# Kernel optimization log

Hardware: AMD Instinct MI355X
Metric: run time of the kernel (lower is better)

The kernel has to match this reference:

```python
import jax, jax.numpy as jnp
import numpy as np

B, CIN, CE, CA, N, S = 2, 64, 128, 128, 1024, 32
SCALE = np.sqrt(np.float32(CA))  # scale_mode == 'dimfts'


def _vnlin(W, x):
    # VNLinear: linear map over the channel dim of (B, C, 3, N, S)
    return jnp.einsum('oc,bcdns->bodns', W, x)


def setup_inputs() -> dict:
    key = jax.random.key(0)
    ks = jax.random.split(key, 16)
    def w(k, o, i):
        return (jax.random.normal(k, (o, i), jnp.float32) / np.sqrt(np.float32(i)))
    return {
        'group_xyz': jax.random.normal(ks[0], (B, N, S, 3), jnp.float32),
        'group_fts': jax.random.normal(ks[1], (B, CIN, 3, N, S), jnp.float32),
        'query_xyz': jax.random.normal(ks[2], (B, N, 3), jnp.float32),
        'W_e1': w(ks[3], CE, CIN), 'W_e2': w(ks[4], CE, CE),
        'W_q': w(ks[5], CA, CE), 'W_k': w(ks[6], CA, CE), 'W_v': w(ks[7], CA, CE),
        'W_r1': w(ks[8], 64, 1), 'W_r2': w(ks[9], CA, 64),
        'W_std': w(ks[10], 3, CA),
        'W_f1': w(ks[11], CA, CA * 3), 'b_f1': jax.random.normal(ks[12], (CA,), jnp.float32) * 0.02,
        'W_f2': w(ks[13], CA, CA), 'b_f2': jax.random.normal(ks[14], (CA,), jnp.float32) * 0.02,
    }


def reference(group_xyz, group_fts, query_xyz, W_e1, W_e2, W_q, W_k, W_v,
              W_r1, W_r2, W_std, W_f1, b_f1, W_f2, b_f2):
    # vnn_e: two stacked VNLinear layers
    group_emb = _vnlin(W_e2, _vnlin(W_e1, group_fts))        # (B, CE, 3, N, S)
    query_emb = group_emb[..., :1]                           # (B, CE, 3, N, 1)
    q = _vnlin(W_q, query_emb)                               # (B, CA, 3, N, 1)
    k = _vnlin(W_k, group_emb)                               # (B, CA, 3, N, S)
    v = _vnlin(W_v, group_emb)                               # (B, CA, 3, N, S)

    # positional relation: xyz_rel -> (B, 1, 3, N, S) -> vnn_r
    xyz_rel = group_xyz - query_xyz[:, :, None, :]           # (B, N, S, 3)
    xyz_rel = jnp.transpose(xyz_rel[:, :, :, None, :], (0, 3, 4, 1, 2))  # (B,1,3,N,S)
    pos_rel = _vnlin(W_r2, _vnlin(W_r1, xyz_rel))            # (B, CA, 3, N, S)

    # relation_func == 'sub'
    attn = q - k + pos_rel                                   # (B, CA, 3, N, S)

    # VNStdFeatureLin (dim=5, no frame normalization): z0 = VNLinear(CA->3)
    z0 = _vnlin(W_std, attn)                                 # (B, 3, 3, N, S)
    attn = jnp.einsum('bijns,bjkns->bikns', attn, z0)        # (B, CA, 3, N, S) invariant

    # attn_fwd: 1x1 conv -> ReLU -> 1x1 conv on (B, CA*3, N, S)
    attn = attn.reshape(B, CA * 3, N, S)
    h = jax.nn.relu(jnp.einsum('oc,bcns->bons', W_f1, attn) + b_f1[:, None, None])
    a = jnp.einsum('oc,bcns->bons', W_f2, h) + b_f2[:, None, None]  # (B, CA, N, S)

    a = jax.nn.softmax(a[:, :, None, :, :] / SCALE, axis=-1)  # (B, CA, 1, N, S)
    v = v + pos_rel
    resi = jnp.sum(a * v, axis=-1)                            # (B, CA, 3, N)
    return resi
```

## Files before the change

kernel.cpp:

```cpp
#include <hip/hip_runtime.h>
#include <hip/hip_bf16.h>
#include <math.h>

typedef __hip_bfloat16  bf16;
typedef __hip_bfloat162 bf162;
typedef __attribute__((ext_vector_type(8))) short short8;
typedef __attribute__((ext_vector_type(4))) float f32x4;

#define BB   2
#define CINC 64
#define NN   1024
#define SSS  32
#define NS   (NN * SSS)

#define OFF_WE21 0
#define OFF_WR   8192
#define OFF_KBA  8320
#define OFF_VB   16512
#define OFF_F1B  20608
#define OFF_F2B  45184
#define WS_NEED_FLOATS 53376

#define S_ATT_B  0
#define S_FTS_B  26112
#define S_XYZ_B  39936
#define SMEM_BYTES 40128

__device__ __forceinline__ float bf2f(short s) {
    unsigned int u = ((unsigned int)(unsigned short)s) << 16;
    return __uint_as_float(u);
}
__device__ __forceinline__ short f2bf(float f) {
    bf16 h = __float2bfloat16(f);
    return *reinterpret_cast<short*>(&h);
}
__device__ __forceinline__ unsigned pk2(float a, float b) {
    bf162 p = __float22bfloat162_rn(make_float2(a, b));
    return *reinterpret_cast<unsigned*>(&p);
}

__global__ __launch_bounds__(256) void prep1(const float* __restrict__ We1,
                                             const float* __restrict__ We2,
                                             float* __restrict__ ws) {
    int e = blockIdx.x * 256 + threadIdx.x;
    int o = e >> 6, c = e & 63;
    float acc = 0.f;
    for (int m = 0; m < 128; ++m)
        acc = fmaf(We2[o * 128 + m], We1[m * 64 + c], acc);
    ws[OFF_WE21 + o * 64 + c] = acc;
}

__global__ __launch_bounds__(256) void prep2(const float* __restrict__ Wq,
                                             const float* __restrict__ Wk,
                                             const float* __restrict__ Wv,
                                             const float* __restrict__ Wr1,
                                             const float* __restrict__ Wr2,
                                             const float* __restrict__ Wf1,
                                             const float* __restrict__ Wf2,
                                             float* __restrict__ ws) {
    const float* we21 = ws + OFF_WE21;
    int e = blockIdx.x * 256 + threadIdx.x;
    if (e < 16384) {
        int i = e >> 7, c2 = e & 127;
        const float* W = (c2 < 64) ? Wk : Wq;
        int c = c2 & 63;
        float acc = 0.f;
        for (int o = 0; o < 128; ++o)
            acc = fmaf(W[i * 128 + o], we21[o * 64 + c], acc);
        if (c2 >= 64) acc = -acc;
        ((bf16*)(ws + OFF_KBA))[i * 128 + c2] = __float2bfloat16(acc);
    } else if (e < 24576) {
        int le = e - 16384;
        int i = le >> 6, c = le & 63;
        float acc = 0.f;
        for (int o = 0; o < 128; ++o)
            acc = fmaf(Wv[i * 128 + o], we21[o * 64 + c], acc);
        ((bf16*)(ws + OFF_VB))[i * 64 + c] = __float2bfloat16(acc);
    } else if (e < 24704) {
        int i = e - 24576;
        float acc = 0.f;
        for (int m = 0; m < 64; ++m)
            acc = fmaf(Wr2[i * 64 + m], Wr1[m], acc);
        ws[OFF_WR + i] = acc;
    } else if (e < 24704 + 49152) {
        int f = e - 24704;
        int o = f / 384, kp = f - o * 384;
        int c = (kp & 127) * 3 + (kp >> 7);
        ((bf16*)(ws + OFF_F1B))[f] = __float2bfloat16(Wf1[o * 384 + c]);
    } else if (e < 24704 + 49152 + 16384) {
        int f = e - (24704 + 49152);
        ((bf16*)(ws + OFF_F2B))[f] = __float2bfloat16(Wf2[f]);
    }
}

__global__ __launch_bounds__(256, 4) void fused_main(
        const float* __restrict__ gxyz, const float* __restrict__ gfts,
        const float* __restrict__ qxyz, const float* __restrict__ Wstd,
        const float* __restrict__ bf1,  const float* __restrict__ bf2,
        const float* __restrict__ ws,   float* __restrict__ out) {
    extern __shared__ char smc[];
    short* s_att  = (short*)(smc + S_ATT_B);
    short* h_t    = s_att;
    short* a_t    = s_att + 4352;
    short* fts_s  = (short*)(smc + S_FTS_B);
    short* s_xyzh = (short*)(smc + S_XYZ_B);
    float* s_red  = (float*)(smc + S_ATT_B);

    const int t    = threadIdx.x;
    const int bid  = blockIdx.x;
    const int b    = bid >> 10;
    const int n    = bid & 1023;
    const int w    = t >> 6;
    const int lane = t & 63;
    const int quad = lane >> 4;
    const int lq   = lane & 15;
    const int wb   = 32 * w;

    const float* gb = gfts + (size_t)b * (CINC * 3 * NS) + n * SSS;
    const short* kba = (const short*)(ws + OFF_KBA);

    short8 Ka[2][2];
    #pragma unroll
    for (int it = 0; it < 2; ++it) {
        int i = wb + it * 16 + lq;
        #pragma unroll
        for (int kc = 0; kc < 2; ++kc)
            Ka[it][kc] = *(const short8*)(kba + i * 128 + kc * 32 + quad * 8);
    }
    float wr2[2] = { ws[OFF_WR + wb + lq], ws[OFF_WR + wb + 16 + lq] };

    #pragma unroll
    for (int h = 0; h < 3; ++h) {
        {
            int cp = t >> 3;
            int ml = (t & 7) * 4;
            const float* fb = gb + (2 * cp * 3 + h) * NS + ml;
            float4 f0 = *(const float4*)(fb);
            float4 f1 = *(const float4*)(fb + 3 * NS);
            short* dst = fts_s + (h * 32 + ml) * 72 + 2 * cp;
            *(unsigned*)(dst)       = pk2(f0.x, f1.x);
            *(unsigned*)(dst + 72)  = pk2(f0.y, f1.y);
            *(unsigned*)(dst + 144) = pk2(f0.z, f1.z);
            *(unsigned*)(dst + 216) = pk2(f0.w, f1.w);
        }
        if (h == 0 && t >= 160) {
            int id = t - 160;
            int d = id >> 5, s = id & 31;
            s_xyzh[id] = f2bf(gxyz[((b * NN + n) * SSS + s) * 3 + d]
                              - qxyz[(b * NN + n) * 3 + d]);
        }
        __syncthreads();

        float qv[2];
        {
            const short* qp = fts_s + (h * 32) * 72 + quad * 8;
            short8 aq0 = *(const short8*)(qp);
            short8 aq1 = *(const short8*)(qp + 32);
            #pragma unroll
            for (int it = 0; it < 2; ++it) {
                int i = wb + it * 16 + lq;
                short8 kq2 = *(const short8*)(kba + i * 128 + 64 + quad * 8);
                short8 kq3 = *(const short8*)(kba + i * 128 + 96 + quad * 8);
                f32x4 qa = {0.f, 0.f, 0.f, 0.f};
                qa = __builtin_amdgcn_mfma_f32_16x16x32_bf16(aq0, kq2, qa, 0, 0, 0);
                qa = __builtin_amdgcn_mfma_f32_16x16x32_bf16(aq1, kq3, qa, 0, 0, 0);
                qv[it] = qa[0];
            }
        }
        #pragma unroll
        for (int mt_h = 0; mt_h < 2; ++mt_h) {
            int mt = h * 2 + mt_h;
            const short* ap = fts_s + (h * 32 + mt_h * 16 + lq) * 72 + quad * 8;
            short8 a0 = *(const short8*)(ap);
            short8 a1 = *(const short8*)(ap + 32);
            #pragma unroll
            for (int it = 0; it < 2; ++it) {
                f32x4 kk = {0.f, 0.f, 0.f, 0.f};
                kk = __builtin_amdgcn_mfma_f32_16x16x32_bf16(a0, Ka[it][0], kk, 0, 0, 0);
                kk = __builtin_amdgcn_mfma_f32_16x16x32_bf16(a1, Ka[it][1], kk, 0, 0, 0);
                int i = wb + it * 16 + lq;
                #pragma unroll
                for (int reg = 0; reg < 4; ++reg) {
                    int m = mt * 16 + quad * 4 + reg;
                    float pos = wr2[it] * bf2f(s_xyzh[m]);
                    s_att[m * 136 + i] = f2bf(pos - kk[reg] - qv[it]);
                }
            }
        }
        __syncthreads();
    }

    {
        short8 As[4];
        #pragma unroll
        for (int kc = 0; kc < 4; ++kc) {
            short8 a = {0, 0, 0, 0, 0, 0, 0, 0};
            if (lq < 3) {
                const float* wp = Wstd + lq * 128 + kc * 32 + quad * 8;
                float4 w0 = *(const float4*)(wp);
                float4 w1 = *(const float4*)(wp + 4);
                a[0] = f2bf(w0.x); a[1] = f2bf(w0.y); a[2] = f2bf(w0.z); a[3] = f2bf(w0.w);
                a[4] = f2bf(w1.x); a[5] = f2bf(w1.y); a[6] = f2bf(w1.z); a[7] = f2bf(w1.w);
            }
            As[kc] = a;
        }
        for (int tile = w; tile < 6; tile += 4) {
            f32x4 acc = {0.f, 0.f, 0.f, 0.f};
            const short* bp = s_att + (tile * 16 + lq) * 136 + quad * 8;
            #pragma unroll
            for (int kc = 0; kc < 4; ++kc) {
                short8 bfr = *(const short8*)(bp + kc * 32);
                acc = __builtin_amdgcn_mfma_f32_16x16x32_bf16(As[kc], bfr, acc, 0, 0, 0);
            }
            if (quad == 0) {
                float* hp = (float*)(fts_s + (tile * 16 + lq) * 72 + 64);
                #pragma unroll
                for (int reg = 0; reg < 3; ++reg)
                    hp[reg] = acc[reg];
            }
        }
    }
    __syncthreads();

    for (int u = t; u < 512; u += 256) {
        int s  = u >> 4;
        int i0 = (u & 15) * 8;
        float z[3][3];
        #pragma unroll
        for (int kk = 0; kk < 3; ++kk) {
            const float* hp = (const float*)(fts_s + (kk * 32 + s) * 72 + 64);
            #pragma unroll
            for (int j = 0; j < 3; ++j)
                z[j][kk] = hp[j];
        }
        float af[3][8];
        #pragma unroll
        for (int j = 0; j < 3; ++j) {
            short8 v8 = *(const short8*)(s_att + (j * 32 + s) * 136 + i0);
            #pragma unroll
            for (int x = 0; x < 8; ++x) af[j][x] = bf2f(v8[x]);
        }
        #pragma unroll
        for (int kk = 0; kk < 3; ++kk) {
            short8 o8;
            #pragma unroll
            for (int x = 0; x < 8; ++x)
                o8[x] = f2bf(af[0][x] * z[0][kk] + af[1][x] * z[1][kk] + af[2][x] * z[2][kk]);
            *(short8*)(s_att + (kk * 32 + s) * 136 + i0) = o8;
        }
    }
    __syncthreads();

    f32x4 eacc[2][2];
    {
        f32x4 zz = {0.f, 0.f, 0.f, 0.f};
        eacc[0][0] = zz; eacc[0][1] = zz; eacc[1][0] = zz; eacc[1][1] = zz;
        const short* f1b = (const short*)(ws + OFF_F1B);
        const short* ab0 = f1b + (wb + lq) * 384 + quad * 8;
        const short* ab1 = ab0 + 16 * 384;
        #pragma unroll 2
        for (int ks = 0; ks < 12; ++ks) {
            int kk = ks >> 2;
            int ic = (ks & 3) * 32 + quad * 8;
            short8 a0 = *(const short8*)(ab0 + ks * 32);
            short8 a1 = *(const short8*)(ab1 + ks * 32);
            const short* bp = s_att + (kk * 32) * 136 + ic;
            short8 b0 = *(const short8*)(bp + lq * 136);
            short8 b1 = *(const short8*)(bp + (lq + 16) * 136);
            eacc[0][0] = __builtin_amdgcn_mfma_f32_16x16x32_bf16(a0, b0, eacc[0][0], 0, 0, 0);
            eacc[0][1] = __builtin_amdgcn_mfma_f32_16x16x32_bf16(a0, b1, eacc[0][1], 0, 0, 0);
            eacc[1][0] = __builtin_amdgcn_mfma_f32_16x16x32_bf16(a1, b0, eacc[1][0], 0, 0, 0);
            eacc[1][1] = __builtin_amdgcn_mfma_f32_16x16x32_bf16(a1, b1, eacc[1][1], 0, 0, 0);
        }
    }
    __syncthreads();

    #pragma unroll
    for (int mt = 0; mt < 2; ++mt) {
        int ob = wb + mt * 16 + quad * 4;
        float4 bb = *(const float4*)(bf1 + ob);
        float bv[4] = {bb.x, bb.y, bb.z, bb.w};
        #pragma unroll
        for (int nt = 0; nt < 2; ++nt) {
            f32x4 c = eacc[mt][nt];
            int s = nt * 16 + lq;
            uint2 pk;
            pk.x = pk2(fmaxf(c[0] + bv[0], 0.f), fmaxf(c[1] + bv[1], 0.f));
            pk.y = pk2(fmaxf(c[2] + bv[2], 0.f), fmaxf(c[3] + bv[3], 0.f));
            *(uint2*)(h_t + s * 136 + ob) = pk;
        }
    }
    __syncthreads();

    {
        f32x4 facc[2][2];
        f32x4 zz = {0.f, 0.f, 0.f, 0.f};
        facc[0][0] = zz; facc[0][1] = zz; facc[1][0] = zz; facc[1][1] = zz;
        const short* f2b = (const short*)(ws + OFF_F2B);
        const short* ab0 = f2b + (wb + lq) * 128 + quad * 8;
        const short* ab1 = ab0 + 16 * 128;
        #pragma unroll 2
        for (int ks = 0; ks < 4; ++ks) {
            int c0 = ks * 32 + quad * 8;
            short8 a0 = *(const short8*)(ab0 + ks * 32);
            short8 a1 = *(const short8*)(ab1 + ks * 32);
            short8 b0 = *(const short8*)(h_t + lq * 136 + c0);
            short8 b1 = *(const short8*)(h_t + (lq + 16) * 136 + c0);
            facc[0][0] = __builtin_amdgcn_mfma_f32_16x16x32_bf16(a0, b0, facc[0][0], 0, 0, 0);
            facc[0][1] = __builtin_amdgcn_mfma_f32_16x16x32_bf16(a0, b1, facc[0][1], 0, 0, 0);
            facc[1][0] = __builtin_amdgcn_mfma_f32_16x16x32_bf16(a1, b0, facc[1][0], 0, 0, 0);
            facc[1][1] = __builtin_amdgcn_mfma_f32_16x16x32_bf16(a1, b1, facc[1][1], 0, 0, 0);
        }
        const float inv = 0.08838834764831845f;
        #pragma unroll
        for (int mt = 0; mt < 2; ++mt) {
            int ob = wb + mt * 16 + quad * 4;
            float4 bb = *(const float4*)(bf2 + ob);
            float bv[4] = {bb.x, bb.y, bb.z, bb.w};
            float a0v[4], a1v[4];
            #pragma unroll
            for (int reg = 0; reg < 4; ++reg) {
                float v0 = facc[mt][0][reg] + bv[reg];
                float v1 = facc[mt][1][reg] + bv[reg];
                float mx = fmaxf(v0, v1);
                mx = fmaxf(mx, __shfl_xor(mx, 1));
                mx = fmaxf(mx, __shfl_xor(mx, 2));
                mx = fmaxf(mx, __shfl_xor(mx, 4));
                mx = fmaxf(mx, __shfl_xor(mx, 8));
                float e0 = __expf((v0 - mx) * inv);
                float e1 = __expf((v1 - mx) * inv);
                float sm = e0 + e1;
                sm += __shfl_xor(sm, 1);
                sm += __shfl_xor(sm, 2);
                sm += __shfl_xor(sm, 4);
                sm += __shfl_xor(sm, 8);
                float rs = 1.f / sm;
                a0v[reg] = e0 * rs;
                a1v[reg] = e1 * rs;
            }
            uint2 pk;
            pk.x = pk2(a0v[0], a0v[1]);
            pk.y = pk2(a0v[2], a0v[3]);
            *(uint2*)(a_t + lq * 136 + ob) = pk;
            pk.x = pk2(a1v[0], a1v[1]);
            pk.y = pk2(a1v[2], a1v[3]);
            *(uint2*)(a_t + (16 + lq) * 136 + ob) = pk;
        }
    }
    __syncthreads();

    {
        __builtin_amdgcn_sched_barrier(0);
        short8 Va[2][2];
        {
            const short* vbb = (const short*)(ws + OFF_VB);
            #pragma unroll
            for (int it = 0; it < 2; ++it) {
                int i = wb + it * 16 + lq;
                #pragma unroll
                for (int kc = 0; kc < 2; ++kc)
                    Va[it][kc] = *(const short8*)(vbb + i * 64 + kc * 32 + quad * 8);
            }
        }
        float pr[2][3];
        #pragma unroll
        for (int it = 0; it < 2; ++it)
            #pragma unroll
            for (int d = 0; d < 3; ++d) pr[it][d] = 0.f;
        #pragma unroll
        for (int mt = 0; mt < 6; ++mt) {
            int d  = mt >> 1;
            int s0 = (mt & 1) * 16 + quad * 4;
            const short* ap = fts_s + (mt * 16 + lq) * 72 + quad * 8;
            short8 a0 = *(const short8*)(ap);
            short8 a1 = *(const short8*)(ap + 32);
            #pragma unroll
            for (int it = 0; it < 2; ++it) {
                f32x4 vv = {0.f, 0.f, 0.f, 0.f};
                vv = __builtin_amdgcn_mfma_f32_16x16x32_bf16(a0, Va[it][0], vv, 0, 0, 0);
                vv = __builtin_amdgcn_mfma_f32_16x16x32_bf16(a1, Va[it][1], vv, 0, 0, 0);
                int i = wb + it * 16 + lq;
                #pragma unroll
                for (int reg = 0; reg < 4; ++reg) {
                    int m = mt * 16 + quad * 4 + reg;
                    float vp = vv[reg] + wr2[it] * bf2f(s_xyzh[m]);
                    pr[it][d] = fmaf(bf2f(a_t[(s0 + reg) * 136 + i]), vp, pr[it][d]);
                }
            }
        }
        #pragma unroll
        for (int it = 0; it < 2; ++it)
            #pragma unroll
            for (int d = 0; d < 3; ++d) {
                float v = pr[it][d];
                v += __shfl_xor(v, 16);
                v += __shfl_xor(v, 32);
                if (quad == 0) s_red[(wb + it * 16 + lq) * 3 + d] = v;
            }
    }
    __syncthreads();

    for (int e = t; e < 384; e += 256)
        out[(b * 384 + e) * NN + n] = s_red[e];
}

extern "C" void kernel_launch(void* const* d_in, const int* in_sizes, int n_in,
                              void* d_out, int out_size, void* d_ws, size_t ws_size,
                              hipStream_t stream) {
    const float* gxyz = (const float*)d_in[0];
    const float* gfts = (const float*)d_in[1];
    const float* qxyz = (const float*)d_in[2];
    const float* We1  = (const float*)d_in[3];
    const float* We2  = (const float*)d_in[4];
    const float* Wq   = (const float*)d_in[5];
    const float* Wk   = (const float*)d_in[6];
    const float* Wv   = (const float*)d_in[7];
    const float* Wr1  = (const float*)d_in[8];
    const float* Wr2  = (const float*)d_in[9];
    const float* Wstd = (const float*)d_in[10];
    const float* bf1  = (const float*)d_in[12];
    const float* bf2  = (const float*)d_in[14];
    float* out = (float*)d_out;
    float* ws  = (float*)d_ws;

    (void)hipFuncSetAttribute((const void*)fused_main,
                              hipFuncAttributeMaxDynamicSharedMemorySize, SMEM_BYTES);

    prep1<<<32, 256, 0, stream>>>(We1, We2, ws);
    prep2<<<353, 256, 0, stream>>>(Wq, Wk, Wv, Wr1, Wr2,
                                   (const float*)d_in[11], (const float*)d_in[13], ws);
    fused_main<<<BB * NN, 256, SMEM_BYTES, stream>>>(gxyz, gfts, qxyz, Wstd,
                                                     bf1, bf2, ws, out);
}
```

Baseline: 177.8 us.

## Prefetch next h-slice of group features and transpose MFMA output for packed stores

Loads the next h-slice of group_fts into registers before the current slice's MFMAs run, and writes it to shared memory afterwards, so global-load latency overlaps with compute. The MFMA operands are swapped so each lane holds four consecutive output channels, and results go to shared memory as one packed 64-bit store instead of four scalar bf16 stores. This also lets the q-projection keep full accumulators rather than one element. It costs extra registers for the prefetched float4s and wr2 vectors, which may lower occupancy.

```diff
diff --git a/kernel.cpp b/kernel.cpp
--- a/kernel.cpp
+++ b/kernel.cpp
@@ -119,6 +119,9 @@
     const float* gb = gfts + (size_t)b * (CINC * 3 * NS) + n * SSS;
     const short* kba = (const short*)(ws + OFF_KBA);
 
+    const int cp = t >> 3;
+    const int ml = (t & 7) * 4;
+
     short8 Ka[2][2];
     #pragma unroll
     for (int it = 0; it < 2; ++it) {
@@ -127,31 +130,38 @@
         for (int kc = 0; kc < 2; ++kc)
             Ka[it][kc] = *(const short8*)(kba + i * 128 + kc * 32 + quad * 8);
     }
+    float4 wr2v[2] = { *(const float4*)(ws + OFF_WR + wb + quad * 4),
+                       *(const float4*)(ws + OFF_WR + wb + 16 + quad * 4) };
     float wr2[2] = { ws[OFF_WR + wb + lq], ws[OFF_WR + wb + 16 + lq] };
 
-    #pragma unroll
-    for (int h = 0; h < 3; ++h) {
-        {
-            int cp = t >> 3;
-            int ml = (t & 7) * 4;
-            const float* fb = gb + (2 * cp * 3 + h) * NS + ml;
-            float4 f0 = *(const float4*)(fb);
-            float4 f1 = *(const float4*)(fb + 3 * NS);
-            short* dst = fts_s + (h * 32 + ml) * 72 + 2 * cp;
-            *(unsigned*)(dst)       = pk2(f0.x, f1.x);
-            *(unsigned*)(dst + 72)  = pk2(f0.y, f1.y);
-            *(unsigned*)(dst + 144) = pk2(f0.z, f1.z);
-            *(unsigned*)(dst + 216) = pk2(f0.w, f1.w);
-        }
-        if (h == 0 && t >= 160) {
+    {
+        const float* fb = gb + (2 * cp * 3 + 0) * NS + ml;
+        float4 f0 = *(const float4*)(fb);
+        float4 f1 = *(const float4*)(fb + 3 * NS);
+        short* dst = fts_s + (0 * 32 + ml) * 72 + 2 * cp;
+        *(unsigned*)(dst)       = pk2(f0.x, f1.x);
+        *(unsigned*)(dst + 72)  = pk2(f0.y, f1.y);
+        *(unsigned*)(dst + 144) = pk2(f0.z, f1.z);
+        *(unsigned*)(dst + 216) = pk2(f0.w, f1.w);
+        if (t >= 160) {
             int id = t - 160;
             int d = id >> 5, s = id & 31;
             s_xyzh[id] = f2bf(gxyz[((b * NN + n) * SSS + s) * 3 + d]
                               - qxyz[(b * NN + n) * 3 + d]);
         }
-        __syncthreads();
-
-        float qv[2];
+    }
+    __syncthreads();
+
+    #pragma unroll
+    for (int h = 0; h < 3; ++h) {
+        float4 g0, g1;
+        if (h < 2) {
+            const float* fb = gb + (2 * cp * 3 + h + 1) * NS + ml;
+            g0 = *(const float4*)(fb);
+            g1 = *(const float4*)(fb + 3 * NS);
+        }
+
+        f32x4 qa[2];
         {
             const short* qp = fts_s + (h * 32) * 72 + quad * 8;
             short8 aq0 = *(const short8*)(qp);
@@ -161,31 +171,41 @@
                 int i = wb + it * 16 + lq;
                 short8 kq2 = *(const short8*)(kba + i * 128 + 64 + quad * 8);
                 short8 kq3 = *(const short8*)(kba + i * 128 + 96 + quad * 8);
-                f32x4 qa = {0.f, 0.f, 0.f, 0.f};
-                qa = __builtin_amdgcn_mfma_f32_16x16x32_bf16(aq0, kq2, qa, 0, 0, 0);
-                qa = __builtin_amdgcn_mfma_f32_16x16x32_bf16(aq1, kq3, qa, 0, 0, 0);
-                qv[it] = qa[0];
+                f32x4 z = {0.f, 0.f, 0.f, 0.f};
+                z = __builtin_amdgcn_mfma_f32_16x16x32_bf16(kq2, aq0, z, 0, 0, 0);
+                z = __builtin_amdgcn_mfma_f32_16x16x32_bf16(kq3, aq1, z, 0, 0, 0);
+                qa[it] = z;
             }
         }
         #pragma unroll
         for (int mt_h = 0; mt_h < 2; ++mt_h) {
-            int mt = h * 2 + mt_h;
-            const short* ap = fts_s + (h * 32 + mt_h * 16 + lq) * 72 + quad * 8;
+            int m = h * 32 + mt_h * 16 + lq;
+            const short* ap = fts_s + m * 72 + quad * 8;
             short8 a0 = *(const short8*)(ap);
             short8 a1 = *(const short8*)(ap + 32);
+            float xm = bf2f(s_xyzh[m]);
             #pragma unroll
             for (int it = 0; it < 2; ++it) {
                 f32x4 kk = {0.f, 0.f, 0.f, 0.f};
-                kk = __builtin_amdgcn_mfma_f32_16x16x32_bf16(a0, Ka[it][0], kk, 0, 0, 0);
-                kk = __builtin_amdgcn_mfma_f32_16x16x32_bf16(a1, Ka[it][1], kk, 0, 0, 0);
-                int i = wb + it * 16 + lq;
+                kk = __builtin_amdgcn_mfma_f32_16x16x32_bf16(Ka[it][0], a0, kk, 0, 0, 0);
+                kk = __builtin_amdgcn_mfma_f32_16x16x32_bf16(Ka[it][1], a1, kk, 0, 0, 0);
+                float p[4];
                 #pragma unroll
-                for (int reg = 0; reg < 4; ++reg) {
-                    int m = mt * 16 + quad * 4 + reg;
-                    float pos = wr2[it] * bf2f(s_xyzh[m]);
-                    s_att[m * 136 + i] = f2bf(pos - kk[reg] - qv[it]);
-                }
-            }
+                for (int reg = 0; reg < 4; ++reg)
+                    p[reg] = wr2v[it][reg] * xm - kk[reg] - qa[it][reg];
+                uint2 pk;
+                pk.x = pk2(p[0], p[1]);
+                pk.y = pk2(p[2], p[3]);
+                *(uint2*)(s_att + m * 136 + wb + it * 16 + quad * 4) = pk;
+            }
+        }
+
+        if (h < 2) {
+            short* dst = fts_s + ((h + 1) * 32 + ml) * 72 + 2 * cp;
+            *(unsigned*)(dst)       = pk2(g0.x, g1.x);
+            *(unsigned*)(dst + 72)  = pk2(g0.y, g1.y);
+            *(unsigned*)(dst + 144) = pk2(g0.z, g1.z);
+            *(unsigned*)(dst + 216) = pk2(g0.w, g1.w);
         }
         __syncthreads();
     }
```

After: 179.2 us. No clear change (+0.8%).
